# Performance work log

Measured on AMD Instinct MI355X. Metric: run time of the kernel, lower is better.

## Reference

```python
import jax, jax.numpy as jnp
import numpy as np

N = 10000        # nodes
E = 160000       # edges
IN = 1024        # in_channels
OUT = 512        # out_channels
H = 2 * OUT      # hidden width of conv1
EPS = 1e-5
NEG_SLOPE = 0.1


def setup_inputs() -> dict:
    key = jax.random.key(0)
    ks = jax.random.split(key, 8)
    s_in = 1.0 / np.sqrt(IN)
    s_h = 1.0 / np.sqrt(H)
    return {
        "x": jax.random.normal(ks[0], (N, IN), jnp.float32),
        "edge_index": jax.random.randint(ks[1], (2, E), 0, N, dtype=jnp.int64),
        "W1": jax.random.normal(ks[2], (IN, H), jnp.float32) * s_in,
        "b1": jnp.zeros((H,), jnp.float32),
        "Wm": jax.random.normal(ks[3], (H, OUT), jnp.float32) * s_h,
        "bm": jnp.zeros((OUT,), jnp.float32),
        "Ws": jax.random.normal(ks[4], (H, OUT), jnp.float32) * s_h,
        "bs": jnp.zeros((OUT,), jnp.float32),
        "gn_weight": jnp.ones((IN,), jnp.float32),
        "gn_bias": jnp.zeros((IN,), jnp.float32),
        "gn_mean_scale": jnp.ones((IN,), jnp.float32),
    }


def reference(x, edge_index, W1, b1, Wm, bm, Ws, bs, gn_weight, gn_bias, gn_mean_scale):
    # --- GraphNorm (eval, single graph: stats over all nodes) ---
    mean = jnp.mean(x, axis=0)                       # [IN]
    xc = x - gn_mean_scale * mean                    # [N, IN]
    var = jnp.mean(xc * xc, axis=0)                  # [IN]
    x = xc * jax.lax.rsqrt(var + EPS) * gn_weight + gn_bias

    # --- GCN normalization: add self loops, symmetric degree norm ---
    loop = jnp.arange(N, dtype=edge_index.dtype)
    src = jnp.concatenate([edge_index[0], loop])     # [E+N]
    dst = jnp.concatenate([edge_index[1], loop])     # [E+N]
    deg = jax.ops.segment_sum(jnp.ones_like(dst, dtype=x.dtype), dst, num_segments=N)
    deg_inv_sqrt = jax.lax.rsqrt(deg)                # deg >= 1 due to self loops
    enorm = deg_inv_sqrt[src] * deg_inv_sqrt[dst]    # [E+N]

    def gcn_conv(h, W, b):
        h = h @ W                                                        # dense GEMM
        agg = jax.ops.segment_sum(h[src] * enorm[:, None], dst, num_segments=N)
        return agg + b

    h = jax.nn.leaky_relu(gcn_conv(x, W1, b1), NEG_SLOPE)                # [N, H]
    mu = gcn_conv(h, Wm, bm)                                             # [N, OUT]
    logstd = gcn_conv(h, Ws, bs)                                         # [N, OUT]
    z = mu  # eval-mode reparametrize returns mu
    return (z, mu, logstd)
```

## Files before the change

kernel.cpp:

```cpp
#include <hip/hip_runtime.h>
#include <hip/hip_bf16.h>
#include <stdint.h>

#define NNODES 10000
#define NEDGES 160000
#define INCH 1024
#define HCH 1024
#define OUTCH 512
#define MPAD 10112
#define EPSV 1e-5f
#define NEG 0.1f

typedef unsigned short u16;
typedef __bf16 bf16x8 __attribute__((ext_vector_type(8)));
typedef float f32x4 __attribute__((ext_vector_type(4)));
typedef __attribute__((address_space(1))) unsigned int gu32;
typedef __attribute__((address_space(3))) unsigned int lu32;

#define GL16(g, l) __builtin_amdgcn_global_load_lds((const gu32*)(g), (lu32*)(l), 16, 0, 0)

__device__ __forceinline__ float bf2f(u16 u) {
    union { unsigned int i; float f; } v; v.i = ((unsigned int)u) << 16; return v.f;
}
__device__ __forceinline__ u16 f2bf(float f) {
    union { float f; unsigned int i; } v; v.f = f;
    unsigned int r = v.i + 0x7fffu + ((v.i >> 16) & 1u);
    return (u16)(r >> 16);
}

__global__ __launch_bounds__(256) void sumsq_k(const float* __restrict__ x,
                                               float* __restrict__ colsum,
                                               float* __restrict__ colsq) {
    int c = threadIdx.x * 4;
    int r0 = blockIdx.x * 16;
    float s0 = 0.f, s1 = 0.f, s2 = 0.f, s3 = 0.f;
    float q0 = 0.f, q1 = 0.f, q2 = 0.f, q3 = 0.f;
#pragma unroll 4
    for (int r = 0; r < 16; ++r) {
        float4 v = *(const float4*)(x + (size_t)(r0 + r) * INCH + c);
        s0 += v.x; s1 += v.y; s2 += v.z; s3 += v.w;
        q0 += v.x * v.x; q1 += v.y * v.y; q2 += v.z * v.z; q3 += v.w * v.w;
    }
    atomicAdd(&colsum[c + 0], s0); atomicAdd(&colsum[c + 1], s1);
    atomicAdd(&colsum[c + 2], s2); atomicAdd(&colsum[c + 3], s3);
    atomicAdd(&colsq[c + 0], q0); atomicAdd(&colsq[c + 1], q1);
    atomicAdd(&colsq[c + 2], q2); atomicAdd(&colsq[c + 3], q3);
}

__global__ void scale_k(const float* __restrict__ colsum, const float* __restrict__ colsq,
                        const float* __restrict__ gms, const float* __restrict__ gw,
                        const float* __restrict__ gb,
                        float* __restrict__ sc, float* __restrict__ sh) {
    int c = blockIdx.x * 256 + threadIdx.x;
    const float invn = 1.0f / NNODES;
    float m = colsum[c] * invn;
    float msq = colsq[c] * invn;
    float g = gms[c];
    float var = msq - g * (2.0f - g) * m * m;
    float s = rsqrtf(var + EPSV) * gw[c];
    sc[c] = s;
    sh[c] = gb[c] - g * m * s;
}

__global__ __launch_bounds__(256) void norm_k(const float* __restrict__ x,
                                              const float* __restrict__ sc,
                                              const float* __restrict__ sh,
                                              u16* __restrict__ xn) {
    int gid = blockIdx.x * 256 + threadIdx.x;
    int e = gid * 4;
    int c = e & (INCH - 1);
    float4 xv = *(const float4*)(x + e);
    float4 s4 = *(const float4*)(sc + c);
    float4 h4 = *(const float4*)(sh + c);
    ushort4 o;
    o.x = f2bf(xv.x * s4.x + h4.x);
    o.y = f2bf(xv.y * s4.y + h4.y);
    o.z = f2bf(xv.z * s4.z + h4.z);
    o.w = f2bf(xv.w * s4.w + h4.w);
    *(ushort4*)(xn + e) = o;
}

__global__ __launch_bounds__(256) void wt1_k(const float* __restrict__ W, u16* __restrict__ Bt) {
    __shared__ u16 t[64][68];
    int k0 = blockIdx.y * 64, c0 = blockIdx.x * 64;
    int tc = (threadIdx.x & 15) * 4;
    int tk = threadIdx.x >> 4;
#pragma unroll
    for (int i = 0; i < 64; i += 16) {
        float4 v = *(const float4*)(W + (size_t)(k0 + tk + i) * HCH + c0 + tc);
        t[tc + 0][tk + i] = f2bf(v.x);
        t[tc + 1][tk + i] = f2bf(v.y);
        t[tc + 2][tk + i] = f2bf(v.z);
        t[tc + 3][tk + i] = f2bf(v.w);
    }
    __syncthreads();
    int wk = (threadIdx.x & 15) * 4;
    int wc = threadIdx.x >> 4;
#pragma unroll
    for (int i = 0; i < 64; i += 16) {
        ushort4 o;
        o.x = t[wc + i][wk + 0]; o.y = t[wc + i][wk + 1];
        o.z = t[wc + i][wk + 2]; o.w = t[wc + i][wk + 3];
        *(ushort4*)(Bt + (size_t)(c0 + wc + i) * 1024 + k0 + wk) = o;
    }
}

__global__ __launch_bounds__(256) void wt2_k(const float* __restrict__ Wm,
                                             const float* __restrict__ Ws,
                                             u16* __restrict__ Bt) {
    __shared__ u16 t[64][68];
    int k0 = blockIdx.y * 64, c0 = blockIdx.x * 64;
    const float* W = (c0 < OUTCH) ? Wm : Ws;
    int cb = (c0 < OUTCH) ? c0 : c0 - OUTCH;
    int tc = (threadIdx.x & 15) * 4;
    int tk = threadIdx.x >> 4;
#pragma unroll
    for (int i = 0; i < 64; i += 16) {
        float4 v = *(const float4*)(W + (size_t)(k0 + tk + i) * OUTCH + cb + tc);
        t[tc + 0][tk + i] = f2bf(v.x);
        t[tc + 1][tk + i] = f2bf(v.y);
        t[tc + 2][tk + i] = f2bf(v.z);
        t[tc + 3][tk + i] = f2bf(v.w);
    }
    __syncthreads();
    int wk = (threadIdx.x & 15) * 4;
    int wc = threadIdx.x >> 4;
#pragma unroll
    for (int i = 0; i < 64; i += 16) {
        ushort4 o;
        o.x = t[wc + i][wk + 0]; o.y = t[wc + i][wk + 1];
        o.z = t[wc + i][wk + 2]; o.w = t[wc + i][wk + 3];
        *(ushort4*)(Bt + (size_t)(c0 + wc + i) * 1024 + k0 + wk) = o;
    }
}

__global__ void deg_k(const int* __restrict__ dst, int* __restrict__ cnt) {
    int e = blockIdx.x * 256 + threadIdx.x;
    if (e < NEDGES) atomicAdd(&cnt[dst[e]], 1);
}
__global__ void dis_k(const int* __restrict__ cnt, float* __restrict__ dis) {
    int i = blockIdx.x * 256 + threadIdx.x;
    if (i < NNODES) dis[i] = rsqrtf((float)(cnt[i] + 1));
}
__global__ void scan_k(const int* __restrict__ cnt, int* __restrict__ row_ptr,
                       int* __restrict__ cursor) {
    __shared__ int sm[256];
    int tid = threadIdx.x;
    const int per = 40;
    int base = tid * per;
    int s = 0;
    for (int i = 0; i < per; ++i) { int idx = base + i; if (idx < NNODES) s += cnt[idx]; }
    sm[tid] = s; __syncthreads();
    for (int off = 1; off < 256; off <<= 1) {
        int v = (tid >= off) ? sm[tid - off] : 0;
        __syncthreads();
        sm[tid] += v;
        __syncthreads();
    }
    int run = (tid == 0) ? 0 : sm[tid - 1];
    for (int i = 0; i < per; ++i) {
        int idx = base + i;
        if (idx < NNODES) { row_ptr[idx] = run; cursor[idx] = run; run += cnt[idx]; }
    }
    if (tid == 255) row_ptr[NNODES] = sm[255];
}
__global__ void fill_k(const int* __restrict__ src, const int* __restrict__ dst,
                       const float* __restrict__ dis, int* __restrict__ cursor,
                       int* __restrict__ csr_src, float* __restrict__ csr_w) {
    int e = blockIdx.x * 256 + threadIdx.x;
    if (e >= NEDGES) return;
    int s = src[e], d = dst[e];
    int pos = atomicAdd(&cursor[d], 1);
    csr_src[pos] = s;
    csr_w[pos] = dis[s] * dis[d];
}

template<int MODE>
__global__ void agg_k(const u16* __restrict__ in, u16* __restrict__ out,
                      const int* __restrict__ row_ptr, const int* __restrict__ csr_src,
                      const float* __restrict__ csr_w, const float* __restrict__ dis,
                      const float* __restrict__ bias) {
    int node = blockIdx.x;
    int c = threadIdx.x * 4;
    float dv = dis[node];
    float selfw = dv * dv;
    ushort4 sv = *(const ushort4*)(in + (size_t)node * HCH + c);
    float a0 = bf2f(sv.x) * selfw, a1 = bf2f(sv.y) * selfw;
    float a2 = bf2f(sv.z) * selfw, a3 = bf2f(sv.w) * selfw;
    int e0 = row_ptr[node], e1 = row_ptr[node + 1];
    for (int e = e0; e < e1; ++e) {
        int s = csr_src[e];
        float w = csr_w[e];
        ushort4 v = *(const ushort4*)(in + (size_t)s * HCH + c);
        a0 += bf2f(v.x) * w; a1 += bf2f(v.y) * w;
        a2 += bf2f(v.z) * w; a3 += bf2f(v.w) * w;
    }
    if (MODE == 1) {
        float4 b = *(const float4*)(bias + c);
        a0 += b.x; a1 += b.y; a2 += b.z; a3 += b.w;
        a0 = a0 > 0.f ? a0 : NEG * a0;
        a1 = a1 > 0.f ? a1 : NEG * a1;
        a2 = a2 > 0.f ? a2 : NEG * a2;
        a3 = a3 > 0.f ? a3 : NEG * a3;
    }
    ushort4 o; o.x = f2bf(a0); o.y = f2bf(a1); o.z = f2bf(a2); o.w = f2bf(a3);
    *(ushort4*)(out + (size_t)node * HCH + c) = o;
}

template<int EPI>
__global__ __launch_bounds__(256) void gemm_k(
    const u16* __restrict__ A, const u16* __restrict__ Bt,
    u16* __restrict__ Cbf, float* __restrict__ out,
    const float* __restrict__ bm, const float* __restrict__ bs) {
    __shared__ u16 As[128 * 32];
    __shared__ u16 Bs[128 * 32];
    const int tid = threadIdx.x;
    const int wave = tid >> 6;
    const int lane = tid & 63;
    const int row0 = blockIdx.y * 128;
    const int col0 = blockIdx.x * 128;
    const int wr = wave >> 1, wc = wave & 1;
    const int sr = lane >> 2;
    const int sc = (lane & 3) * 8;
    u16* AsW0 = &As[(wave * 16) * 32];
    u16* AsW1 = &As[(64 + wave * 16) * 32];
    u16* BsW0 = &Bs[(wave * 16) * 32];
    u16* BsW1 = &Bs[(64 + wave * 16) * 32];
    const u16* Ag0 = A + (size_t)(row0 + wave * 16 + sr) * 1024 + sc;
    const u16* Ag1 = A + (size_t)(row0 + 64 + wave * 16 + sr) * 1024 + sc;
    const u16* Bg0 = Bt + (size_t)(col0 + wave * 16 + sr) * 1024 + sc;
    const u16* Bg1 = Bt + (size_t)(col0 + 64 + wave * 16 + sr) * 1024 + sc;

    f32x4 acc[4][4] = {};
    const int arow = lane & 15;
    const int ak = (lane >> 4) * 8;
    for (int kk = 0; kk < 1024; kk += 32) {
        GL16(Ag0 + kk, AsW0);
        GL16(Ag1 + kk, AsW1);
        GL16(Bg0 + kk, BsW0);
        GL16(Bg1 + kk, BsW1);
        __syncthreads();
        bf16x8 af[4], bf[4];
#pragma unroll
        for (int m = 0; m < 4; ++m)
            af[m] = *reinterpret_cast<const bf16x8*>(&As[(wr * 64 + m * 16 + arow) * 32 + ak]);
#pragma unroll
        for (int n = 0; n < 4; ++n)
            bf[n] = *reinterpret_cast<const bf16x8*>(&Bs[(wc * 64 + n * 16 + arow) * 32 + ak]);
#pragma unroll
        for (int m = 0; m < 4; ++m)
#pragma unroll
            for (int n = 0; n < 4; ++n)
                acc[m][n] = __builtin_amdgcn_mfma_f32_16x16x32_bf16(af[m], bf[n], acc[m][n], 0, 0, 0);
        __syncthreads();
    }
    const int crow = (lane >> 4) * 4;
    const int ccol = lane & 15;
    if (EPI == 0) {
#pragma unroll
        for (int m = 0; m < 4; ++m) {
            int rbase = row0 + wr * 64 + m * 16 + crow;
#pragma unroll
            for (int n = 0; n < 4; ++n) {
                int col = col0 + wc * 64 + n * 16 + ccol;
                f32x4 v = acc[m][n];
#pragma unroll
                for (int r = 0; r < 4; ++r)
                    Cbf[(size_t)(rbase + r) * 1024 + col] = f2bf(v[r]);
            }
        }
    } else {
        const size_t NOUT = (size_t)NNODES * OUTCH;
#pragma unroll
        for (int n = 0; n < 4; ++n) {
            int col = col0 + wc * 64 + n * 16 + ccol;
            bool lo = col < OUTCH;
            int colo = lo ? col : col - OUTCH;
            float bias = lo ? bm[colo] : bs[colo];
#pragma unroll
            for (int m = 0; m < 4; ++m) {
                int rbase = row0 + wr * 64 + m * 16 + crow;
                f32x4 v = acc[m][n];
#pragma unroll
                for (int r = 0; r < 4; ++r) {
                    int rr = rbase + r;
                    if (rr < NNODES) {
                        float val = v[r] + bias;
                        if (lo) {
                            out[(size_t)rr * OUTCH + colo] = val;
                            out[NOUT + (size_t)rr * OUTCH + colo] = val;
                        } else {
                            out[2 * NOUT + (size_t)rr * OUTCH + colo] = val;
                        }
                    }
                }
            }
        }
    }
}

extern "C" void kernel_launch(void* const* d_in, const int* in_sizes, int n_in,
                              void* d_out, int out_size, void* d_ws, size_t ws_size,
                              hipStream_t stream) {
    const float* x   = (const float*)d_in[0];
    const int*   ei  = (const int*)d_in[1];
    const float* W1  = (const float*)d_in[2];
    const float* b1  = (const float*)d_in[3];
    const float* Wm  = (const float*)d_in[4];
    const float* bm  = (const float*)d_in[5];
    const float* Ws  = (const float*)d_in[6];
    const float* bs  = (const float*)d_in[7];
    const float* gw  = (const float*)d_in[8];
    const float* gb  = (const float*)d_in[9];
    const float* gms = (const float*)d_in[10];
    const int* srcI = ei;
    const int* dstI = ei + NEDGES;

    char* ws = (char*)d_ws;
    const size_t SBIG = (size_t)MPAD * 1024 * 2;
    u16* xn   = (u16*)(ws);
    u16* h1g  = (u16*)(ws + SBIG);
    u16* h    = (u16*)(ws + 2 * SBIG);
    u16* aggh = xn;
    u16* Bt1  = (u16*)(ws + 3 * SBIG);
    u16* Bt2  = (u16*)(ws + 3 * SBIG + (size_t)2 * 1024 * 1024);
    char* small   = ws + 3 * SBIG + (size_t)4 * 1024 * 1024;
    float* colsum = (float*)(small);
    float* colsq  = (float*)(small + 4096);
    int*   cnt    = (int*)(small + 8192);
    int*   row_ptr= (int*)(small + 49152);
    int*   cursor = (int*)(small + 49152 + 40960);
    float* dis    = (float*)(small + 49152 + 81920);
    int*   csr_src= (int*)(small + 49152 + 122880);
    float* csr_w  = (float*)(small + 49152 + 122880 + 640000);
    float* sc     = (float*)(small + 49152 + 122880 + 1280000);
    float* sh     = (float*)(small + 49152 + 122880 + 1280000 + 4096);

    hipMemsetAsync(small, 0, 48192, stream);

    sumsq_k<<<625, 256, 0, stream>>>(x, colsum, colsq);
    scale_k<<<4, 256, 0, stream>>>(colsum, colsq, gms, gw, gb, sc, sh);
    norm_k<<<10000, 256, 0, stream>>>(x, sc, sh, xn);
    wt1_k<<<dim3(16, 16), 256, 0, stream>>>(W1, Bt1);
    wt2_k<<<dim3(16, 16), 256, 0, stream>>>(Wm, Ws, Bt2);
    deg_k<<<625, 256, 0, stream>>>(dstI, cnt);
    dis_k<<<40, 256, 0, stream>>>(cnt, dis);
    scan_k<<<1, 256, 0, stream>>>(cnt, row_ptr, cursor);
    fill_k<<<625, 256, 0, stream>>>(srcI, dstI, dis, cursor, csr_src, csr_w);

    gemm_k<0><<<dim3(8, 79), 256, 0, stream>>>(xn, Bt1, h1g, nullptr, nullptr, nullptr);
    agg_k<1><<<NNODES, 256, 0, stream>>>(h1g, h, row_ptr, csr_src, csr_w, dis, b1);
    agg_k<0><<<NNODES, 256, 0, stream>>>(h, aggh, row_ptr, csr_src, csr_w, dis, nullptr);
    gemm_k<1><<<dim3(8, 79), 256, 0, stream>>>(aggh, Bt2, nullptr, (float*)d_out, bm, bs);
}
```

Baseline: 415.1 us.

## Fold GraphNorm affine into W1 and a per-node bias correction

Rather than normalising x before the first GEMM, the code casts raw x to bf16 and computes the column statistics from that bf16 copy. The per-column scale is folded into W1 during its transpose. The shift becomes a vector c1 = sh·W1, added in the first aggregation weighted by each node's row sum of normalised edge weights. This removes one full read pass over the fp32 x. The cost is two extra small kernels and atomics, plus some precision loss: statistics come from bf16 values, and the un-centred raw x goes into the GEMM, so the shift term cancels against it afterwards.

Measured after the change: 434.4 us. +4.6%, slower.

```diff
diff --git a/kernel.cpp b/kernel.cpp
--- a/kernel.cpp
+++ b/kernel.cpp
@@ -28,18 +28,29 @@
     return (u16)(r >> 16);
 }
 
-__global__ __launch_bounds__(256) void sumsq_k(const float* __restrict__ x,
+__global__ __launch_bounds__(256) void cast_k(const float* __restrict__ x,
+                                              u16* __restrict__ xn) {
+    int gid = blockIdx.x * 256 + threadIdx.x;
+    int e = gid * 4;
+    float4 v = *(const float4*)(x + e);
+    ushort4 o;
+    o.x = f2bf(v.x); o.y = f2bf(v.y); o.z = f2bf(v.z); o.w = f2bf(v.w);
+    *(ushort4*)(xn + e) = o;
+}
+
+__global__ __launch_bounds__(256) void sumsq_k(const u16* __restrict__ xn,
                                                float* __restrict__ colsum,
                                                float* __restrict__ colsq) {
     int c = threadIdx.x * 4;
     int r0 = blockIdx.x * 16;
     float s0 = 0.f, s1 = 0.f, s2 = 0.f, s3 = 0.f;
     float q0 = 0.f, q1 = 0.f, q2 = 0.f, q3 = 0.f;
-#pragma unroll 4
+#pragma unroll
     for (int r = 0; r < 16; ++r) {
-        float4 v = *(const float4*)(x + (size_t)(r0 + r) * INCH + c);
-        s0 += v.x; s1 += v.y; s2 += v.z; s3 += v.w;
-        q0 += v.x * v.x; q1 += v.y * v.y; q2 += v.z * v.z; q3 += v.w * v.w;
+        ushort4 v = *(const ushort4*)(xn + (size_t)(r0 + r) * INCH + c);
+        float f0 = bf2f(v.x), f1 = bf2f(v.y), f2 = bf2f(v.z), f3 = bf2f(v.w);
+        s0 += f0; s1 += f1; s2 += f2; s3 += f3;
+        q0 += f0 * f0; q1 += f1 * f1; q2 += f2 * f2; q3 += f3 * f3;
     }
     atomicAdd(&colsum[c + 0], s0); atomicAdd(&colsum[c + 1], s1);
     atomicAdd(&colsum[c + 2], s2); atomicAdd(&colsum[c + 3], s3);
@@ -62,36 +73,31 @@
     sh[c] = gb[c] - g * m * s;
 }
 
-__global__ __launch_bounds__(256) void norm_k(const float* __restrict__ x,
-                                              const float* __restrict__ sc,
-                                              const float* __restrict__ sh,
-                                              u16* __restrict__ xn) {
-    int gid = blockIdx.x * 256 + threadIdx.x;
-    int e = gid * 4;
-    int c = e & (INCH - 1);
-    float4 xv = *(const float4*)(x + e);
-    float4 s4 = *(const float4*)(sc + c);
-    float4 h4 = *(const float4*)(sh + c);
-    ushort4 o;
-    o.x = f2bf(xv.x * s4.x + h4.x);
-    o.y = f2bf(xv.y * s4.y + h4.y);
-    o.z = f2bf(xv.z * s4.z + h4.z);
-    o.w = f2bf(xv.w * s4.w + h4.w);
-    *(ushort4*)(xn + e) = o;
-}
-
-__global__ __launch_bounds__(256) void wt1_k(const float* __restrict__ W, u16* __restrict__ Bt) {
+__global__ void c1_k(const float* __restrict__ W1, const float* __restrict__ sh,
+                     float* __restrict__ c1) {
+    int j = blockIdx.x * 256 + threadIdx.x;
+    int k0 = blockIdx.y * 128;
+    float a = 0.f;
+#pragma unroll 4
+    for (int k = k0; k < k0 + 128; ++k) a += sh[k] * W1[(size_t)k * HCH + j];
+    atomicAdd(&c1[j], a);
+}
+
+__global__ __launch_bounds__(256) void wt1_k(const float* __restrict__ W,
+                                             const float* __restrict__ sc,
+                                             u16* __restrict__ Bt) {
     __shared__ u16 t[64][68];
     int k0 = blockIdx.y * 64, c0 = blockIdx.x * 64;
     int tc = (threadIdx.x & 15) * 4;
     int tk = threadIdx.x >> 4;
 #pragma unroll
     for (int i = 0; i < 64; i += 16) {
+        float scr = sc[k0 + tk + i];
         float4 v = *(const float4*)(W + (size_t)(k0 + tk + i) * HCH + c0 + tc);
-        t[tc + 0][tk + i] = f2bf(v.x);
-        t[tc + 1][tk + i] = f2bf(v.y);
-        t[tc + 2][tk + i] = f2bf(v.z);
-        t[tc + 3][tk + i] = f2bf(v.w);
+        t[tc + 0][tk + i] = f2bf(v.x * scr);
+        t[tc + 1][tk + i] = f2bf(v.y * scr);
+        t[tc + 2][tk + i] = f2bf(v.z * scr);
+        t[tc + 3][tk + i] = f2bf(v.w * scr);
     }
     __syncthreads();
     int wk = (threadIdx.x & 15) * 4;
@@ -138,9 +144,14 @@
     int e = blockIdx.x * 256 + threadIdx.x;
     if (e < NEDGES) atomicAdd(&cnt[dst[e]], 1);
 }
-__global__ void dis_k(const int* __restrict__ cnt, float* __restrict__ dis) {
+__global__ void dis_k(const int* __restrict__ cnt, float* __restrict__ dis,
+                      float* __restrict__ rowsum) {
     int i = blockIdx.x * 256 + threadIdx.x;
-    if (i < NNODES) dis[i] = rsqrtf((float)(cnt[i] + 1));
+    if (i < NNODES) {
+        float d = rsqrtf((float)(cnt[i] + 1));
+        dis[i] = d;
+        rowsum[i] = d * d;
+    }
 }
 __global__ void scan_k(const int* __restrict__ cnt, int* __restrict__ row_ptr,
                        int* __restrict__ cursor) {
@@ -166,20 +177,24 @@
 }
 __global__ void fill_k(const int* __restrict__ src, const int* __restrict__ dst,
                        const float* __restrict__ dis, int* __restrict__ cursor,
-                       int* __restrict__ csr_src, float* __restrict__ csr_w) {
+                       int* __restrict__ csr_src, float* __restrict__ csr_w,
+                       float* __restrict__ rowsum) {
     int e = blockIdx.x * 256 + threadIdx.x;
     if (e >= NEDGES) return;
     int s = src[e], d = dst[e];
+    float w = dis[s] * dis[d];
     int pos = atomicAdd(&cursor[d], 1);
     csr_src[pos] = s;
-    csr_w[pos] = dis[s] * dis[d];
+    csr_w[pos] = w;
+    atomicAdd(&rowsum[d], w);
 }
 
 template<int MODE>
 __global__ void agg_k(const u16* __restrict__ in, u16* __restrict__ out,
                       const int* __restrict__ row_ptr, const int* __restrict__ csr_src,
                       const float* __restrict__ csr_w, const float* __restrict__ dis,
-                      const float* __restrict__ bias) {
+                      const float* __restrict__ bias, const float* __restrict__ rowsum,
+                      const float* __restrict__ c1) {
     int node = blockIdx.x;
     int c = threadIdx.x * 4;
     float dv = dis[node];
@@ -196,8 +211,11 @@
         a2 += bf2f(v.z) * w; a3 += bf2f(v.w) * w;
     }
     if (MODE == 1) {
+        float rs = rowsum[node];
         float4 b = *(const float4*)(bias + c);
-        a0 += b.x; a1 += b.y; a2 += b.z; a3 += b.w;
+        float4 cc = *(const float4*)(c1 + c);
+        a0 += rs * cc.x + b.x; a1 += rs * cc.y + b.y;
+        a2 += rs * cc.z + b.z; a3 += rs * cc.w + b.w;
         a0 = a0 > 0.f ? a0 : NEG * a0;
         a1 = a1 > 0.f ? a1 : NEG * a1;
         a2 = a2 > 0.f ? a2 : NEG * a2;
@@ -328,28 +346,31 @@
     float* colsum = (float*)(small);
     float* colsq  = (float*)(small + 4096);
     int*   cnt    = (int*)(small + 8192);
-    int*   row_ptr= (int*)(small + 49152);
-    int*   cursor = (int*)(small + 49152 + 40960);
-    float* dis    = (float*)(small + 49152 + 81920);
-    int*   csr_src= (int*)(small + 49152 + 122880);
-    float* csr_w  = (float*)(small + 49152 + 122880 + 640000);
-    float* sc     = (float*)(small + 49152 + 122880 + 1280000);
-    float* sh     = (float*)(small + 49152 + 122880 + 1280000 + 4096);
-
-    hipMemsetAsync(small, 0, 48192, stream);
-
-    sumsq_k<<<625, 256, 0, stream>>>(x, colsum, colsq);
+    float* rowsum = (float*)(small + 49152);
+    float* c1     = (float*)(small + 90112);
+    int*   row_ptr= (int*)(small + 94208);
+    int*   cursor = (int*)(small + 135168);
+    float* dis    = (float*)(small + 176128);
+    int*   csr_src= (int*)(small + 217088);
+    float* csr_w  = (float*)(small + 857088);
+    float* sc     = (float*)(small + 1497088);
+    float* sh     = (float*)(small + 1501184);
+
+    hipMemsetAsync(small, 0, 94208, stream);
+
+    cast_k<<<10000, 256, 0, stream>>>(x, xn);
+    deg_k<<<625, 256, 0, stream>>>(dstI, cnt);
+    dis_k<<<40, 256, 0, stream>>>(cnt, dis, rowsum);
+    scan_k<<<1, 256, 0, stream>>>(cnt, row_ptr, cursor);
+    fill_k<<<625, 256, 0, stream>>>(srcI, dstI, dis, cursor, csr_src, csr_w, rowsum);
+    sumsq_k<<<625, 256, 0, stream>>>(xn, colsum, colsq);
     scale_k<<<4, 256, 0, stream>>>(colsum, colsq, gms, gw, gb, sc, sh);
-    norm_k<<<10000, 256, 0, stream>>>(x, sc, sh, xn);
-    wt1_k<<<dim3(16, 16), 256, 0, stream>>>(W1, Bt1);
+    wt1_k<<<dim3(16, 16), 256, 0, stream>>>(W1, sc, Bt1);
+    c1_k<<<dim3(4, 8), 256, 0, stream>>>(W1, sh, c1);
     wt2_k<<<dim3(16, 16), 256, 0, stream>>>(Wm, Ws, Bt2);
-    deg_k<<<625, 256, 0, stream>>>(dstI, cnt);
-    dis_k<<<40, 256, 0, stream>>>(cnt, dis);
-    scan_k<<<1, 256, 0, stream>>>(cnt, row_ptr, cursor);
-    fill_k<<<625, 256, 0, stream>>>(srcI, dstI, dis, cursor, csr_src, csr_w);
 
     gemm_k<0><<<dim3(8, 79), 256, 0, stream>>>(xn, Bt1, h1g, nullptr, nullptr, nullptr);
-    agg_k<1><<<NNODES, 256, 0, stream>>>(h1g, h, row_ptr, csr_src, csr_w, dis, b1);
-    agg_k<0><<<NNODES, 256, 0, stream>>>(h, aggh, row_ptr, csr_src, csr_w, dis, nullptr);
+    agg_k<1><<<NNODES, 256, 0, stream>>>(h1g, h, row_ptr, csr_src, csr_w, dis, b1, rowsum, c1);
+    agg_k<0><<<NNODES, 256, 0, stream>>>(h, aggh, row_ptr, csr_src, csr_w, dis, nullptr, nullptr, nullptr);
     gemm_k<1><<<dim3(8, 79), 256, 0, stream>>>(aggh, Bt2, nullptr, (float*)d_out, bm, bs);
 }
```
